# Kernel optimization log

Hardware: AMD Instinct MI355X
Metric: run time of the kernel (lower is better)

Reference implementation:

```python
import jax, jax.numpy as jnp
import numpy as np


def setup_inputs() -> dict:
    key = jax.random.key(0)
    k1, k2 = jax.random.split(key)
    flow = jax.random.normal(k1, (4, 2, 256, 256), dtype=jnp.float32)   # [B,2,H,W] per-pixel flow over dt
    spike = jax.random.uniform(k2, (4, 64, 256, 256), dtype=jnp.float32)  # [B,C,H,W] spike voxel grid
    return {"flow": flow, "spike": spike}


def _splat(vals, xn, yn, H, W):
    """Forward bilinear splat of vals [H,W] to continuous coords (xn,yn) [H,W]."""
    x0 = jnp.floor(xn)
    y0 = jnp.floor(yn)
    wx = xn - x0  # fractional weights (differentiable w.r.t. flow)
    wy = yn - y0
    x0i = x0.astype(jnp.int32)
    y0i = y0.astype(jnp.int32)
    out = jnp.zeros(H * W, dtype=vals.dtype)
    corners = (
        (0, 0, (1.0 - wx) * (1.0 - wy)),
        (1, 0, wx * (1.0 - wy)),
        (0, 1, (1.0 - wx) * wy),
        (1, 1, wx * wy),
    )
    for dx, dy, w in corners:
        xi = x0i + dx
        yi = y0i + dy
        valid = (xi >= 0) & (xi < W) & (yi >= 0) & (yi < H)
        idx = jnp.clip(yi, 0, H - 1) * W + jnp.clip(xi, 0, W - 1)
        out = out.at[idx.ravel()].add(jnp.where(valid, w * vals, 0.0).ravel())
    return out.reshape(H, W)


def spike_warp_mid(spike, flow, dt):
    """Warp each time bin c by flow * (c - mid)/dt toward the middle timestamp (bilinear splat)."""
    B, C, H, W = spike.shape
    mid = (C - 1) / 2.0
    yy, xx = jnp.meshgrid(jnp.arange(H, dtype=spike.dtype),
                          jnp.arange(W, dtype=spike.dtype), indexing='ij')
    s = (jnp.arange(C, dtype=spike.dtype) - mid) / jnp.asarray(dt, spike.dtype)  # [C]
    u = flow[:, 0][:, None]  # [B,1,H,W]
    v = flow[:, 1][:, None]
    xn = xx + u * s[None, :, None, None]  # [B,C,H,W]
    yn = yy + v * s[None, :, None, None]
    splat_bc = jax.vmap(jax.vmap(lambda va, xa, ya: _splat(va, xa, ya, H, W)))
    return splat_bc(spike, xn, yn)  # [B,C,H,W]


def reference(flow, spike):
    B, C, H, W = spike.shape
    spike_warped = spike_warp_mid(spike, flow, dt=64)
    # Faithful to original: sum over BATCH dim inside per-batch loop (same each iter),
    # so loss = (B * -var) / B = -var(spike_image) with unbiased variance.
    spike_image = jnp.sum(spike_warped, axis=0)  # [C,H,W]
    loss = -jnp.var(spike_image - jnp.mean(spike_image), ddof=1)
    return loss
```

## Files before the change

kernel.cpp:

```cpp
#include <hip/hip_runtime.h>

constexpr int B = 4, C = 64, H = 256, W = 256;
constexpr int HW = H * W;
constexpr long long N_TOT = (long long)C * HW;

constexpr int TS = 16;
constexpr int R = 4;
constexpr int SW = 24;
constexpr int PS = 25;
constexpr int SAREA = SW * SW;
constexpr int NBLK = 256 * 8;

__global__ __launch_bounds__(256) void fused_kernel(
    const float* __restrict__ flow,
    const float* __restrict__ spike,
    double* __restrict__ partials) {
  __shared__ float2 uv[SW * PS];
  __shared__ float4 spkA[SW * PS];
  __shared__ float4 spkB[SW * PS];
  __shared__ int2 rowmax[2][SW];
  __shared__ double red[8];

  const int bid = blockIdx.x;
  const int tile = bid & 255;
  const int j = bid >> 8;
  const int tx0 = (tile & 15) * TS;
  const int ty0 = (tile >> 4) * TS;
  const int tid = threadIdx.x;
  const int qx = tid & 15, qy = tid >> 4;
  const int wave = tid >> 6;

  float smag[4];
#pragma unroll
  for (int t = 0; t < 4; ++t)
    smag[t] = ((float)(4 * j + t) + 0.5f) * (1.0f / 64.0f);
  const int cn0 = 31 - 4 * j;
  const int cp0 = 32 + 4 * j;

  float acc[8];
#pragma unroll
  for (int t = 0; t < 8; ++t) acc[t] = 0.f;

  bool c_act[3], c_val[3];
  int c_apos[3], c_row[3], c_gp[3];
#pragma unroll
  for (int k = 0; k < 3; ++k) {
    int pos = tid + 256 * k;
    c_act[k] = pos < SAREA;
    int row = pos / SW;
    int col = pos - row * SW;
    c_apos[k] = row * PS + col;
    c_row[k] = row;
    int gy = ty0 + row - R, gx = tx0 + col - R;
    c_val[k] = c_act[k] & ((unsigned)gy < (unsigned)H) & ((unsigned)gx < (unsigned)W);
    c_gp[k] = gy * W + gx;
  }

  float p_u[3], p_v[3];
  float4 p_a[3], p_b[3];

  auto prefetch = [&](int b) {
    const float* fu = flow + (size_t)b * 2 * HW;
    const float* fv = fu + HW;
    const float* spb = spike + (size_t)b * C * HW;
#pragma unroll
    for (int k = 0; k < 3; ++k) {
      float u = 0.f, v = 0.f;
      float4 a = {0.f, 0.f, 0.f, 0.f};
      float4 d = {0.f, 0.f, 0.f, 0.f};
      if (c_val[k]) {
        int gp = c_gp[k];
        u = fu[gp];
        v = fv[gp];
        a.x = spb[(size_t)cn0 * HW + gp];
        a.y = spb[(size_t)(cn0 - 1) * HW + gp];
        a.z = spb[(size_t)(cn0 - 2) * HW + gp];
        a.w = spb[(size_t)(cn0 - 3) * HW + gp];
        d.x = spb[(size_t)cp0 * HW + gp];
        d.y = spb[(size_t)(cp0 + 1) * HW + gp];
        d.z = spb[(size_t)(cp0 + 2) * HW + gp];
        d.w = spb[(size_t)(cp0 + 3) * HW + gp];
      }
      p_u[k] = u; p_v[k] = v; p_a[k] = a; p_b[k] = d;
    }
  };

  auto store_lds = [&](int b) {
    int bs = b & 1;
#pragma unroll
    for (int k = 0; k < 3; ++k) {
      if (c_act[k]) {
        int ap = c_apos[k];
        uv[ap] = make_float2(p_u[k], p_v[k]);
        spkA[ap] = p_a[k];
        spkB[ap] = p_b[k];
        atomicMax(&rowmax[bs][c_row[k]].x, __float_as_int(fabsf(p_u[k])));
        atomicMax(&rowmax[bs][c_row[k]].y, __float_as_int(fabsf(p_v[k])));
      }
    }
  };

  if (tid < SW) {
    rowmax[0][tid] = make_int2(0, 0);
    rowmax[1][tid] = make_int2(0, 0);
  }
  prefetch(0);
  __syncthreads();

  const int qpos = (qy + R) * PS + (qx + R);
  const int wr0 = 4 * wave;

  for (int b = 0; b < B; ++b) {
    store_lds(b);
    __syncthreads();

    int mu = 0, mv = 0;
#pragma unroll
    for (int i = 0; i < 12; ++i) {
      int2 rmv = rowmax[b & 1][wr0 + i];
      mu = max(mu, rmv.x);
      mv = max(mv, rmv.y);
    }
    float fmu = __int_as_float(mu), fmv = __int_as_float(mv);
    int rx = min((int)(1.0f + fmu * smag[3]), R);
    int ry = min((int)(1.0f + fmv * smag[3]), R);

    if (b + 1 < B) prefetch(b + 1);

    for (int dy = -ry; dy <= ry; ++dy) {
      float fdy = (float)dy;
      for (int dx = -rx; dx <= rx; ++dx) {
        int pp = qpos + dy * PS + dx;
        float2 u2 = uv[pp];
        float4 va = spkA[pp];
        float4 vb = spkB[pp];
        float fdx = (float)dx;
        const float* vaf = &va.x;
        const float* vbf = &vb.x;
#pragma unroll
        for (int t = 0; t < 4; ++t) {
          float sm = smag[t];
          float txn = fmaxf(0.f, 1.f - fabsf(fmaf(u2.x, -sm, fdx)));
          float tyn = fmaxf(0.f, 1.f - fabsf(fmaf(u2.y, -sm, fdy)));
          acc[t] = fmaf(txn * tyn, vaf[t], acc[t]);
          float txp = fmaxf(0.f, 1.f - fabsf(fmaf(u2.x, sm, fdx)));
          float typ = fmaxf(0.f, 1.f - fabsf(fmaf(u2.y, sm, fdy)));
          acc[4 + t] = fmaf(txp * typ, vbf[t], acc[4 + t]);
        }
      }
    }

    if (tid < SW) rowmax[(b + 1) & 1][tid] = make_int2(0, 0);
    __syncthreads();
  }

  double ls = 0.0, lq = 0.0;
#pragma unroll
  for (int t = 0; t < 8; ++t) {
    double a = (double)acc[t];
    ls += a;
    lq += a * a;
  }
  for (int off = 32; off > 0; off >>= 1) {
    ls += __shfl_down(ls, off, 64);
    lq += __shfl_down(lq, off, 64);
  }
  if ((tid & 63) == 0) { red[wave * 2] = ls; red[wave * 2 + 1] = lq; }
  __syncthreads();
  if (tid == 0) {
    partials[2 * bid] = red[0] + red[2] + red[4] + red[6];
    partials[2 * bid + 1] = red[1] + red[3] + red[5] + red[7];
  }
}

__global__ __launch_bounds__(256) void finalize_kernel(
    const double* __restrict__ partials, float* __restrict__ out) {
  double s = 0.0, q = 0.0;
  for (int i = threadIdx.x; i < NBLK; i += 256) {
    s += partials[2 * i];
    q += partials[2 * i + 1];
  }
  for (int off = 32; off > 0; off >>= 1) {
    s += __shfl_down(s, off, 64);
    q += __shfl_down(q, off, 64);
  }
  __shared__ double ss[4], qq[4];
  int lane = threadIdx.x & 63;
  int wave = threadIdx.x >> 6;
  if (lane == 0) { ss[wave] = s; qq[wave] = q; }
  __syncthreads();
  if (threadIdx.x == 0) {
    double sum = ss[0] + ss[1] + ss[2] + ss[3];
    double sq = qq[0] + qq[1] + qq[2] + qq[3];
    double n = (double)N_TOT;
    double var = (sq - sum * sum / n) / (n - 1.0);
    out[0] = (float)(-var);
  }
}

extern "C" void kernel_launch(void* const* d_in, const int* in_sizes, int n_in,
                              void* d_out, int out_size, void* d_ws, size_t ws_size,
                              hipStream_t stream) {
  const float* flow = (const float*)d_in[0];
  const float* spike = (const float*)d_in[1];
  float* out = (float*)d_out;
  double* partials = (double*)d_ws;

  fused_kernel<<<dim3(NBLK), dim3(256), 0, stream>>>(flow, spike, partials);
  finalize_kernel<<<1, dim3(256), 0, stream>>>(partials, out);
}
```

Before: 164.7 us.

## Pack gather math into float2 vectors and use block-wide flow max

Rewrites the inner gather loop to use float2 vector arithmetic, pairing each negative-time bin with its positive-time mirror so packed FMA instructions can process both at once. Spike values are re-laid out in LDS as interleaved (neg, pos) pairs without row padding. The per-row atomicMax bound search is replaced by a shuffle-plus-LDS block-wide max, which gives a coarser (tile-wide) search radius for every wave. That removes LDS atomics but may enlarge the loop bounds for some waves, and the unpadded layout can introduce LDS bank conflicts.

```diff
diff --git a/kernel.cpp b/kernel.cpp
--- a/kernel.cpp
+++ b/kernel.cpp
@@ -1,4 +1,6 @@
 #include <hip/hip_runtime.h>
+
+typedef float f2 __attribute__((ext_vector_type(2)));
 
 constexpr int B = 4, C = 64, H = 256, W = 256;
 constexpr int HW = H * W;
@@ -7,7 +9,6 @@
 constexpr int TS = 16;
 constexpr int R = 4;
 constexpr int SW = 24;
-constexpr int PS = 25;
 constexpr int SAREA = SW * SW;
 constexpr int NBLK = 256 * 8;
 
@@ -15,10 +16,9 @@
     const float* __restrict__ flow,
     const float* __restrict__ spike,
     double* __restrict__ partials) {
-  __shared__ float2 uv[SW * PS];
-  __shared__ float4 spkA[SW * PS];
-  __shared__ float4 spkB[SW * PS];
-  __shared__ int2 rowmax[2][SW];
+  __shared__ f2 uv[SAREA];
+  __shared__ f2 spk[SAREA * 4];
+  __shared__ float wmx[4], wmy[4];
   __shared__ double red[8];
 
   const int bid = blockIdx.x;
@@ -30,27 +30,30 @@
   const int qx = tid & 15, qy = tid >> 4;
   const int wave = tid >> 6;
 
-  float smag[4];
-#pragma unroll
-  for (int t = 0; t < 4; ++t)
-    smag[t] = ((float)(4 * j + t) + 0.5f) * (1.0f / 64.0f);
+  f2 smv[4];
+  float smag3;
+#pragma unroll
+  for (int t = 0; t < 4; ++t) {
+    float sm = ((float)(4 * j + t) + 0.5f) * (1.0f / 64.0f);
+    smv[t] = f2{-sm, sm};
+    if (t == 3) smag3 = sm;
+  }
   const int cn0 = 31 - 4 * j;
   const int cp0 = 32 + 4 * j;
 
-  float acc[8];
-#pragma unroll
-  for (int t = 0; t < 8; ++t) acc[t] = 0.f;
+  f2 acc2[4];
+#pragma unroll
+  for (int t = 0; t < 4; ++t) acc2[t] = f2{0.f, 0.f};
 
   bool c_act[3], c_val[3];
-  int c_apos[3], c_row[3], c_gp[3];
+  int c_apos[3], c_gp[3];
 #pragma unroll
   for (int k = 0; k < 3; ++k) {
     int pos = tid + 256 * k;
     c_act[k] = pos < SAREA;
     int row = pos / SW;
     int col = pos - row * SW;
-    c_apos[k] = row * PS + col;
-    c_row[k] = row;
+    c_apos[k] = pos;
     int gy = ty0 + row - R, gx = tx0 + col - R;
     c_val[k] = c_act[k] & ((unsigned)gy < (unsigned)H) & ((unsigned)gx < (unsigned)W);
     c_gp[k] = gy * W + gx;
@@ -85,81 +88,67 @@
     }
   };
 
-  auto store_lds = [&](int b) {
-    int bs = b & 1;
+  prefetch(0);
+
+  const int qpos = (qy + R) * SW + (qx + R);
+
+  for (int b = 0; b < B; ++b) {
+    float mu = 0.f, mv = 0.f;
 #pragma unroll
     for (int k = 0; k < 3; ++k) {
       if (c_act[k]) {
         int ap = c_apos[k];
-        uv[ap] = make_float2(p_u[k], p_v[k]);
-        spkA[ap] = p_a[k];
-        spkB[ap] = p_b[k];
-        atomicMax(&rowmax[bs][c_row[k]].x, __float_as_int(fabsf(p_u[k])));
-        atomicMax(&rowmax[bs][c_row[k]].y, __float_as_int(fabsf(p_v[k])));
+        uv[ap] = f2{p_u[k], p_v[k]};
+        f2* sp = &spk[ap * 4];
+        sp[0] = f2{p_a[k].x, p_b[k].x};
+        sp[1] = f2{p_a[k].y, p_b[k].y};
+        sp[2] = f2{p_a[k].z, p_b[k].z};
+        sp[3] = f2{p_a[k].w, p_b[k].w};
+        mu = fmaxf(mu, fabsf(p_u[k]));
+        mv = fmaxf(mv, fabsf(p_v[k]));
       }
     }
-  };
-
-  if (tid < SW) {
-    rowmax[0][tid] = make_int2(0, 0);
-    rowmax[1][tid] = make_int2(0, 0);
-  }
-  prefetch(0);
-  __syncthreads();
-
-  const int qpos = (qy + R) * PS + (qx + R);
-  const int wr0 = 4 * wave;
-
-  for (int b = 0; b < B; ++b) {
-    store_lds(b);
+    for (int off = 32; off > 0; off >>= 1) {
+      mu = fmaxf(mu, __shfl_down(mu, off, 64));
+      mv = fmaxf(mv, __shfl_down(mv, off, 64));
+    }
+    if ((tid & 63) == 0) { wmx[wave] = mu; wmy[wave] = mv; }
     __syncthreads();
-
-    int mu = 0, mv = 0;
-#pragma unroll
-    for (int i = 0; i < 12; ++i) {
-      int2 rmv = rowmax[b & 1][wr0 + i];
-      mu = max(mu, rmv.x);
-      mv = max(mv, rmv.y);
-    }
-    float fmu = __int_as_float(mu), fmv = __int_as_float(mv);
-    int rx = min((int)(1.0f + fmu * smag[3]), R);
-    int ry = min((int)(1.0f + fmv * smag[3]), R);
+    float bu = fmaxf(fmaxf(wmx[0], wmx[1]), fmaxf(wmx[2], wmx[3]));
+    float bv = fmaxf(fmaxf(wmy[0], wmy[1]), fmaxf(wmy[2], wmy[3]));
+    int rx = min((int)(1.0f + bu * smag3), R);
+    int ry = min((int)(1.0f + bv * smag3), R);
 
     if (b + 1 < B) prefetch(b + 1);
 
     for (int dy = -ry; dy <= ry; ++dy) {
-      float fdy = (float)dy;
+      const f2 fdy2 = (float)dy;
       for (int dx = -rx; dx <= rx; ++dx) {
-        int pp = qpos + dy * PS + dx;
-        float2 u2 = uv[pp];
-        float4 va = spkA[pp];
-        float4 vb = spkB[pp];
-        float fdx = (float)dx;
-        const float* vaf = &va.x;
-        const float* vbf = &vb.x;
+        const int pp = qpos + dy * SW + dx;
+        f2 u2 = uv[pp];
+        const f2* vp = &spk[pp * 4];
+        const f2 fdx2 = (float)dx;
+        const f2 ux = f2{u2.x, u2.x};
+        const f2 vy = f2{u2.y, u2.y};
 #pragma unroll
         for (int t = 0; t < 4; ++t) {
-          float sm = smag[t];
-          float txn = fmaxf(0.f, 1.f - fabsf(fmaf(u2.x, -sm, fdx)));
-          float tyn = fmaxf(0.f, 1.f - fabsf(fmaf(u2.y, -sm, fdy)));
-          acc[t] = fmaf(txn * tyn, vaf[t], acc[t]);
-          float txp = fmaxf(0.f, 1.f - fabsf(fmaf(u2.x, sm, fdx)));
-          float typ = fmaxf(0.f, 1.f - fabsf(fmaf(u2.y, sm, fdy)));
-          acc[4 + t] = fmaf(txp * typ, vbf[t], acc[4 + t]);
+          f2 ax = __builtin_elementwise_fma(ux, smv[t], fdx2);
+          f2 ay = __builtin_elementwise_fma(vy, smv[t], fdy2);
+          f2 tx = __builtin_elementwise_max(1.0f - __builtin_elementwise_abs(ax), f2{0.f, 0.f});
+          f2 ty = __builtin_elementwise_max(1.0f - __builtin_elementwise_abs(ay), f2{0.f, 0.f});
+          acc2[t] = __builtin_elementwise_fma(tx * ty, vp[t], acc2[t]);
         }
       }
     }
-
-    if (tid < SW) rowmax[(b + 1) & 1][tid] = make_int2(0, 0);
     __syncthreads();
   }
 
   double ls = 0.0, lq = 0.0;
 #pragma unroll
-  for (int t = 0; t < 8; ++t) {
-    double a = (double)acc[t];
-    ls += a;
-    lq += a * a;
+  for (int t = 0; t < 4; ++t) {
+    double a = (double)acc2[t].x, b2 = (double)acc2[t].y;
+    ls += a + b2;
+    lq += a * a + b2 * b2;
   }
   for (int off = 32; off > 0; off >>= 1) {
     ls += __shfl_down(ls, off, 64);
```

Result: faster. 156.5 us (-5.0%).
